# Optimization experiments

Hardware: AMD Instinct MI355X
Metric: run time of the kernel (lower is better)

The kernel has to match this reference:

```python
import jax, jax.numpy as jnp
import numpy as np

# ---- static config (mirrors module init / config constants) ----
STATE_DIM = 512
D_H = 2048
INPUT_DIM = 1024
N_QUBITS = 6
N_VQC_LAYERS = 3
MSD = 128                 # mamba_state_dim (last dim of padded state)
PAD_SLICES = 16           # padded slice count in h_padded
MIN_T = 1e-6              # control_limits.min_value
REL_STEP = 0.1            # control_limits.hardware_relative_step
ABS_STEP = 1e-4           # control_limits.hardware_absolute_step
MAX_T = 0.05              # control_limits.max_value
DIM = 2 ** N_QUBITS

# qubit 0 = most significant bit (matches reshape-based gate application)
_BITS = ((np.arange(DIM)[:, None] >> np.arange(N_QUBITS)[None, ::-1]) & 1).astype(np.float32)
_sign = np.ones(DIM, np.float32)
for k in range(N_QUBITS):  # ring CZ entanglement
    k2 = (k + 1) % N_QUBITS
    _sign *= 1.0 - 2.0 * _BITS[:, k] * _BITS[:, k2]
CZ_SIGN = jnp.asarray(_sign)
Z_OBS = jnp.asarray((1.0 - 2.0 * _BITS).mean(axis=1))  # mean <Z_k> observable weights


def _apply_ry(state, ang, k):
    # state: [B, 2^n] real statevector; ang: [B] rotation angle on qubit k
    B = state.shape[0]
    s = state.reshape(B, 2 ** k, 2, 2 ** (N_QUBITS - k - 1))
    c = jnp.cos(ang / 2)[:, None, None]
    si = jnp.sin(ang / 2)[:, None, None]
    a0, a1 = s[:, :, 0, :], s[:, :, 1, :]
    out = jnp.stack([c * a0 - si * a1, si * a0 + c * a1], axis=2)
    return out.reshape(B, DIM)


def _vqc(feats, enc_W, enc_b, thetas):
    # EvolutionTimeVQCLayer: angle-encode features, layered RY + ring CZ, mean-Z expectation
    B = feats.shape[0]
    angles = feats @ enc_W + enc_b  # [B, n_qubits]
    state = jnp.zeros((B, DIM), feats.dtype).at[:, 0].set(1.0)
    for k in range(N_QUBITS):
        state = _apply_ry(state, angles[:, k], k)
    for l in range(N_VQC_LAYERS):
        for k in range(N_QUBITS):
            state = _apply_ry(state, jnp.broadcast_to(thetas[l, k], (B,)), k)
        state = state * CZ_SIGN[None, :]
    return (state * state) @ Z_OBS  # [B]


def _hamiltonian(q, p, x, W1, b1, W2, b2, W3, b3):
    z = jnp.concatenate([q, p, x], axis=-1)          # [B, 2*S + D]
    h1 = jnp.tanh(z @ W1 + b1)
    h2 = jnp.tanh(h1 @ W2 + b2)
    return (h2 @ W3)[:, 0] + b3                       # [B] scalar energy per sample


def setup_inputs() -> dict:
    key = jax.random.key(0)
    ks = jax.random.split(key, 12)
    def glorot(k, shape):
        std = np.sqrt(2.0 / (shape[0] + shape[-1]))
        return jax.random.normal(k, shape, jnp.float32) * std
    B = 2048
    h_in = 2 * STATE_DIM + INPUT_DIM
    gen_in = INPUT_DIM + 2 * STATE_DIM
    return {
        'x': jax.random.normal(ks[0], (B, INPUT_DIM), jnp.float32),
        'h_padded': jax.random.normal(ks[1], (B, PAD_SLICES, MSD), jnp.float32),
        'aux_padded': jnp.zeros((B, PAD_SLICES, MSD), jnp.float32),
        'W1': glorot(ks[2], (h_in, D_H)), 'b1': jnp.zeros((D_H,), jnp.float32),
        'W2': glorot(ks[3], (D_H, D_H)), 'b2': jnp.zeros((D_H,), jnp.float32),
        'W3': glorot(ks[4], (D_H, 1)), 'b3': jnp.zeros((), jnp.float32),
        'W_out': glorot(ks[5], (2 * STATE_DIM, INPUT_DIM)),
        'b_out': jnp.zeros((INPUT_DIM,), jnp.float32),
        'enc_W': glorot(ks[6], (gen_in, N_QUBITS)) * 0.1,
        'enc_b': jnp.zeros((N_QUBITS,), jnp.float32),
        'thetas': jax.random.normal(ks[7], (N_VQC_LAYERS, N_QUBITS), jnp.float32) * 0.1,
        'gain': jnp.asarray(0.1, jnp.float32),
        'shift': jnp.asarray(7.0, jnp.float32),
        'cap_param': jnp.asarray(0.02, jnp.float32),
        'time_bias': jnp.asarray(0.0005, jnp.float32),
        'last_stable': jnp.asarray(0.0005, jnp.float32),
    }


def reference(x, h_padded, aux_padded, W1, b1, W2, b2, W3, b3, W_out, b_out,
              enc_W, enc_b, thetas, gain, shift, cap_param, time_bias, last_stable):
    B = x.shape[0]
    total = 2 * STATE_DIM
    num_slices = total // MSD
    # unpack phase-space state from padded mamba-shaped state
    unpacked = h_padded[:, :num_slices, :].reshape(B, total)
    q_t, p_t = jnp.split(unpacked, 2, axis=-1)

    # ---- evolution-time generation via VQC ----
    ctrl = jnp.concatenate([x, q_t, p_t], axis=-1)
    samples = _vqc(ctrl, enc_W, enc_b, thetas)                       # [B]
    soft_gain = jax.nn.softplus(gain)
    soft_shift = jax.nn.softplus(shift)
    adjusted = jax.nn.softplus(soft_gain * samples - soft_shift)
    raw = jnp.mean(adjusted) + time_bias
    cap = jnp.maximum(jax.nn.softplus(cap_param), 1e-6)
    evo = cap * jax.nn.sigmoid(raw / cap)
    evo = jnp.where(jnp.isfinite(evo), evo, cap * jax.nn.sigmoid(time_bias / cap))
    prev = jnp.maximum(last_stable, MIN_T)
    cand = jnp.maximum(evo, MIN_T)
    max_step = jnp.maximum(prev * REL_STEP, ABS_STEP)
    cand = jnp.minimum(cand, prev + max_step)
    cand = jnp.minimum(cand, MAX_T)
    dt = jnp.where(jnp.isfinite(cand), cand, prev)                   # scalar

    # ---- fused HNN symplectic (leapfrog) step ----
    def H_sum(q, p):
        return _hamiltonian(q, p, x, W1, b1, W2, b2, W3, b3).sum()
    grad_qp = jax.grad(H_sum, argnums=(0, 1))
    dHdq0, _ = grad_qp(q_t, p_t)
    p_half = p_t - 0.5 * dt * dHdq0
    _, dHdp_h = grad_qp(q_t, p_half)
    q_next = q_t + dt * dHdp_h
    dHdq_n, _ = grad_qp(q_next, p_half)
    p_next = p_half - 0.5 * dt * dHdq_n

    out = jnp.concatenate([q_next, p_next], axis=-1) @ W_out + b_out  # [B, INPUT_DIM]

    # repack state into padded mamba layout
    new_slices = jnp.concatenate([q_next, p_next], axis=-1).reshape(B, num_slices, MSD)
    pad = jnp.zeros((B, PAD_SLICES - num_slices, MSD), out.dtype)
    h_next = jnp.concatenate([new_slices, pad], axis=1)
    return out, h_next
```

## Files before the change

kernel.cpp:

```cpp
#include <hip/hip_runtime.h>
#include <math.h>

#define NB 2048
#define ZD 2048
#define SD 512
#define NELEM_Z (NB * ZD)
#define MB_ (1024 * 1024)

typedef float f32x4 __attribute__((ext_vector_type(4)));
typedef __bf16 bf16x8 __attribute__((ext_vector_type(8)));
typedef __bf16 bf16x4 __attribute__((ext_vector_type(4)));
typedef int i32x4 __attribute__((ext_vector_type(4)));
typedef int i32x8 __attribute__((ext_vector_type(8)));
typedef long long i64;

__device__ __forceinline__ float softplus_f(float x) {
  if (x > 20.f) return x;
  if (x < -20.f) return expf(x);
  return log1pf(expf(x));
}

__device__ __forceinline__ void gload_lds16(const __bf16* g, __bf16* l) {
  __builtin_amdgcn_global_load_lds(
      (__attribute__((address_space(1))) void*)(g),
      (__attribute__((address_space(3))) void*)(l), 16, 0, 0);
}

__device__ __forceinline__ int pack_fp8x4(float a, float b, float c, float d) {
  int p = __builtin_amdgcn_cvt_pk_fp8_f32(a, b, 0, false);
  p = __builtin_amdgcn_cvt_pk_fp8_f32(c, d, p, true);
  return p;
}
__device__ __forceinline__ float fp8_to_f32(unsigned char b) {
  return __builtin_amdgcn_cvt_f32_fp8((int)b, 0);
}

__global__ __launch_bounds__(256) void build_z_kernel(
    const float* __restrict__ x,
    const float* __restrict__ h_padded,
    const float* __restrict__ enc_W,
    const float* __restrict__ enc_b,
    float* __restrict__ z,
    __bf16* __restrict__ zb,
    unsigned char* __restrict__ zf8,
    float* __restrict__ angles) {
  int b = blockIdx.x;
  int tid = threadIdx.x;
  int lane = tid & 63, w = tid >> 6;
  __shared__ float red[4][6];

  float pa[6] = {0.f, 0.f, 0.f, 0.f, 0.f, 0.f};
#pragma unroll
  for (int cc = 0; cc < 2; cc++) {
    int c = cc * 256 + tid;
    int i = c * 4;
    f32x4 v = (i < 1024) ? ((const f32x4*)(h_padded + (size_t)b * 2048))[c]
                         : ((const f32x4*)(x + (size_t)b * 1024))[c - 256];
    size_t zi = (size_t)b * 512 + c;
    if (cc == 0) {
      ((f32x4*)z)[zi] = v;
      bf16x4 o;
      o[0] = (__bf16)v[0]; o[1] = (__bf16)v[1];
      o[2] = (__bf16)v[2]; o[3] = (__bf16)v[3];
      ((bf16x4*)zb)[zi] = o;
    }
    ((int*)zf8)[zi] = pack_fp8x4(v[0], v[1], v[2], v[3]);
    int cj = (i < 1024) ? (1024 + i) : (i - 1024);
#pragma unroll
    for (int e = 0; e < 4; e++) {
      const float* wp = enc_W + (size_t)(cj + e) * 6;
#pragma unroll
      for (int k = 0; k < 6; k++) pa[k] += v[e] * wp[k];
    }
  }
#pragma unroll
  for (int k = 0; k < 6; k++)
    for (int off = 32; off > 0; off >>= 1) pa[k] += __shfl_down(pa[k], off, 64);
  if (lane == 0) {
#pragma unroll
    for (int k = 0; k < 6; k++) red[w][k] = pa[k];
  }
  __syncthreads();
  if (tid < 6)
    angles[b * 6 + tid] =
        red[0][tid] + red[1][tid] + red[2][tid] + red[3][tid] + enc_b[tid];
}

__global__ void prep_w(const float* __restrict__ in,
                       __bf16* __restrict__ outT, int R, int C) {
  __shared__ float tile[32][33];
  int bx = blockIdx.x * 32, by = blockIdx.y * 32;
  int tx = threadIdx.x, ty = threadIdx.y;
  for (int r = ty; r < 32; r += 8)
    tile[r][tx] = in[(size_t)(by + r) * C + bx + tx];
  __syncthreads();
  for (int r = ty; r < 32; r += 8)
    outT[(size_t)(bx + r) * R + by + tx] = (__bf16)tile[tx][r];
}

__global__ void prep_w8(const float* __restrict__ in,
                        unsigned char* __restrict__ outN,
                        unsigned char* __restrict__ outT, int R, int C) {
  __shared__ float tile[32][33];
  int bx = blockIdx.x * 32, by = blockIdx.y * 32;
  int tx = threadIdx.x, ty = threadIdx.y;
  for (int r = ty; r < 32; r += 8) {
    float v = in[(size_t)(by + r) * C + bx + tx] * 16.f;
    tile[r][tx] = v;
    int p = __builtin_amdgcn_cvt_pk_fp8_f32(v, v, 0, false);
    outN[(size_t)(by + r) * C + bx + tx] = (unsigned char)(p & 0xff);
  }
  __syncthreads();
  for (int r = ty; r < 32; r += 8) {
    float v = tile[tx][r];
    int p = __builtin_amdgcn_cvt_pk_fp8_f32(v, v, 0, false);
    outT[(size_t)(bx + r) * R + by + tx] = (unsigned char)(p & 0xff);
  }
}

__global__ __launch_bounds__(256) void sim_kernel(
    const float* __restrict__ angles,
    const float* __restrict__ thetas,
    const float* __restrict__ gain,
    const float* __restrict__ shift,
    float* __restrict__ partial) {
  const int lane = threadIdx.x & 63;
  const int wv = threadIdx.x >> 6;
  const int row = blockIdx.x * 4 + wv;

  const int rot = ((lane << 1) | (lane >> 5)) & 63;
  const float czs = (__popc(lane & rot) & 1) ? -1.f : 1.f;
  const float zo = (6.f - 2.f * (float)__popc(lane)) * (1.f / 6.f);

  float ang = 0.f;
  if (lane < 6) ang = angles[row * 6 + lane];
  else if (lane < 24) ang = thetas[lane - 6];
  float half = 0.5f * ang;
  float cj = cosf(half), sj = sinf(half);

  float c_arr[24], s_arr[24];
#pragma unroll
  for (int j = 0; j < 24; j++) {
    c_arr[j] = __shfl(cj, j, 64);
    s_arr[j] = __shfl(sj, j, 64);
  }

  float s = (lane == 0) ? 1.f : 0.f;
#pragma unroll
  for (int j = 0; j < 24; j++) {
    const int m = 1 << (5 - (j % 6));
    float t = __shfl_xor(s, m, 64);
    float tt = (lane & m) ? t : -t;
    s = fmaf(c_arr[j], s, s_arr[j] * tt);
    if (j >= 6 && (j % 6) == 5) s *= czs;
  }

  float val = s * s * zo;
#pragma unroll
  for (int off = 32; off > 0; off >>= 1) val += __shfl_xor(val, off, 64);

  __shared__ float red[4];
  if (lane == 0) {
    float sg = softplus_f(gain[0]);
    float ss = softplus_f(shift[0]);
    red[wv] = softplus_f(sg * val - ss);
  }
  __syncthreads();
  if (threadIdx.x == 0)
    partial[blockIdx.x] = red[0] + red[1] + red[2] + red[3];
}

__global__ __launch_bounds__(256) void dt_kernel(
    const float* __restrict__ partial,
    const float* __restrict__ cap_param,
    const float* __restrict__ time_bias,
    const float* __restrict__ last_stable,
    float* __restrict__ dt_out) {
  int tid = threadIdx.x;
  int lane = tid & 63, wv = tid >> 6;
  float v = partial[tid] + partial[tid + 256];
#pragma unroll
  for (int off = 32; off > 0; off >>= 1) v += __shfl_xor(v, off, 64);
  __shared__ float red[4];
  if (lane == 0) red[wv] = v;
  __syncthreads();
  if (tid == 0) {
    float a = red[0] + red[1] + red[2] + red[3];
    float raw = a * (1.f / (float)NB) + time_bias[0];
    float cap = fmaxf(softplus_f(cap_param[0]), 1e-6f);
    float evo = cap / (1.f + expf(-raw / cap));
    if (!isfinite(evo)) evo = cap / (1.f + expf(-time_bias[0] / cap));
    float prev = fmaxf(last_stable[0], 1e-6f);
    float cand = fmaxf(evo, 1e-6f);
    float max_step = fmaxf(prev * 0.1f, 1e-4f);
    cand = fminf(cand, prev + max_step);
    cand = fminf(cand, 0.05f);
    dt_out[0] = isfinite(cand) ? cand : prev;
  }
}

template <int EPI>
__global__ __launch_bounds__(256, 2) void mfma_gemm8(
    const unsigned char* __restrict__ A, int lda,
    const unsigned char* __restrict__ Bt, int ldb,
    void* __restrict__ Cv, int ldc,
    const float* __restrict__ bias,
    const float* __restrict__ w3,
    const unsigned char* __restrict__ aux, int ldaux,
    int Kslice) {
  __shared__ __align__(16) unsigned char sA[2][128 * 128];
  __shared__ __align__(16) unsigned char sB[2][64 * 128];

  const int tid = threadIdx.x;
  const int lane = tid & 63;
  const int w = tid >> 6;
  const int wm = w & 1, wn = w >> 1;
  const int row0 = blockIdx.y * 128;
  const int col0 = blockIdx.x * 64;
  const int koff = blockIdx.z * Kslice;

  const unsigned char* gA[4]; int wA[4];
  const unsigned char* gB[2]; int wB[2];
#pragma unroll
  for (int i = 0; i < 4; i++) {
    int c = i * 256 + tid;
    int m = c >> 3, s = c & 7;
    gA[i] = A + (size_t)(row0 + m) * lda + koff + s * 16;
    wA[i] = m * 128 + ((s ^ (m & 7)) << 4);
  }
#pragma unroll
  for (int i = 0; i < 2; i++) {
    int c = i * 256 + tid;
    int m = c >> 3, s = c & 7;
    gB[i] = Bt + (size_t)(col0 + m) * ldb + koff + s * 16;
    wB[i] = m * 128 + ((s ^ (m & 7)) << 4);
  }

  const int q = lane >> 4, r = lane & 15;
  int aoff[4][2], boff[2][2];
#pragma unroll
  for (int i = 0; i < 4; i++) {
    int ma = wm * 64 + i * 16 + r;
#pragma unroll
    for (int H = 0; H < 2; H++)
      aoff[i][H] = ma * 128 + (((2 * q + H) ^ (ma & 7)) << 4);
  }
#pragma unroll
  for (int j = 0; j < 2; j++) {
    int mb = wn * 32 + j * 16 + r;
#pragma unroll
    for (int H = 0; H < 2; H++)
      boff[j][H] = mb * 128 + (((2 * q + H) ^ (mb & 7)) << 4);
  }

  f32x4 acc[4][2] = {};
  f32x4 rA[4], rB[2];

#pragma unroll
  for (int i = 0; i < 4; i++) rA[i] = *(const f32x4*)gA[i];
#pragma unroll
  for (int i = 0; i < 2; i++) rB[i] = *(const f32x4*)gB[i];
#pragma unroll
  for (int i = 0; i < 4; i++) *(f32x4*)(&sA[0][0] + wA[i]) = rA[i];
#pragma unroll
  for (int i = 0; i < 2; i++) *(f32x4*)(&sB[0][0] + wB[i]) = rB[i];
  __syncthreads();

  int cur = 0;
  for (int k0 = 0; k0 < Kslice; k0 += 128) {
    const bool more = (k0 + 128 < Kslice);
    if (more) {
#pragma unroll
      for (int i = 0; i < 4; i++) rA[i] = *(const f32x4*)(gA[i] + k0 + 128);
#pragma unroll
      for (int i = 0; i < 2; i++) rB[i] = *(const f32x4*)(gB[i] + k0 + 128);
    }

    const unsigned char* bA = &sA[cur][0];
    const unsigned char* bB = &sB[cur][0];
    i32x8 af[4], bfr[2];
#pragma unroll
    for (int i = 0; i < 4; i++) {
      i32x4 lo = *(const i32x4*)(bA + aoff[i][0]);
      i32x4 hi = *(const i32x4*)(bA + aoff[i][1]);
      af[i] = __builtin_shufflevector(lo, hi, 0, 1, 2, 3, 4, 5, 6, 7);
    }
#pragma unroll
    for (int j = 0; j < 2; j++) {
      i32x4 lo = *(const i32x4*)(bB + boff[j][0]);
      i32x4 hi = *(const i32x4*)(bB + boff[j][1]);
      bfr[j] = __builtin_shufflevector(lo, hi, 0, 1, 2, 3, 4, 5, 6, 7);
    }
#pragma unroll
    for (int i = 0; i < 4; i++)
#pragma unroll
      for (int j = 0; j < 2; j++)
        acc[i][j] = __builtin_amdgcn_mfma_scale_f32_16x16x128_f8f6f4(
            af[i], bfr[j], acc[i][j], 0 , 0 ,
            0, 0x7F7F7F7F, 0, 0x7F7F7F7F);

    if (more) {
      unsigned char* nA = &sA[cur ^ 1][0];
      unsigned char* nB = &sB[cur ^ 1][0];
#pragma unroll
      for (int i = 0; i < 4; i++) *(f32x4*)(nA + wA[i]) = rA[i];
#pragma unroll
      for (int i = 0; i < 2; i++) *(f32x4*)(nB + wB[i]) = rB[i];
    }
    __syncthreads();
    cur ^= 1;
  }

  float* Cf = (float*)Cv;
  unsigned char* C8 = (unsigned char*)Cv;
  float* Pz = Cf + (size_t)blockIdx.z * (size_t)gridDim.y * 128 * ldc;

#pragma unroll
  for (int i = 0; i < 4; i++) {
    int rowb = row0 + wm * 64 + i * 16 + q * 4;
#pragma unroll
    for (int j = 0; j < 2; j++) {
      int col = col0 + wn * 32 + j * 16 + r;
      if (EPI == 0) {
#pragma unroll
        for (int g = 0; g < 4; g++)
          Pz[(size_t)(rowb + g) * ldc + col] = acc[i][j][g];
      } else {
        float o[4];
#pragma unroll
        for (int g = 0; g < 4; g++) {
          float v = acc[i][j][g] * 0.0625f;
          if (EPI == 1) {
            o[g] = tanhf(v + bias[col]);
          } else if (EPI == 2) {
            float t = tanhf(v + bias[col]);
            o[g] = 32.f * (1.f - t * t) * w3[col];
          } else {
            float h = fp8_to_f32(aux[(size_t)(rowb + g) * ldaux + col]);
            o[g] = v * (1.f - h * h);
          }
        }
        int p = pack_fp8x4(o[0], o[1], o[2], o[3]);
#pragma unroll
        for (int g = 0; g < 4; g++)
          C8[(size_t)(rowb + g) * ldc + col] =
              (unsigned char)((p >> (8 * g)) & 0xff);
      }
    }
  }
}

__global__ __launch_bounds__(256, 2) void mfma_gemm_bf16(
    const __bf16* __restrict__ A, int lda,
    const __bf16* __restrict__ Bt, int ldb,
    float* __restrict__ P, int ldc,
    int Kslice) {
  __shared__ __bf16 sA[2][128 * 64];
  __shared__ __bf16 sB[2][64 * 64];

  const int tid = threadIdx.x;
  const int lane = tid & 63;
  const int w = tid >> 6;
  const int wm = w & 1, wn = w >> 1;
  const int row0 = blockIdx.y * 128;
  const int col0 = blockIdx.x * 64;
  const int koff = blockIdx.z * Kslice;

  const __bf16* gA[4]; int lofA[4];
  const __bf16* gB[2]; int lofB[2];
#pragma unroll
  for (int i = 0; i < 4; i++) {
    int c = i * 256 + tid;
    int m = c >> 3, cc = c & 7;
    int o = cc ^ (m & 7);
    gA[i] = A + (size_t)(row0 + m) * lda + koff + o * 8;
    lofA[i] = c * 8;
  }
#pragma unroll
  for (int i = 0; i < 2; i++) {
    int c = i * 256 + tid;
    int m = c >> 3, cc = c & 7;
    int o = cc ^ (m & 7);
    gB[i] = Bt + (size_t)(col0 + m) * ldb + koff + o * 8;
    lofB[i] = c * 8;
  }

  const int q = lane >> 4, r = lane & 15;
  int aoff[4][2], boff[2][2];
#pragma unroll
  for (int i = 0; i < 4; i++) {
    int ma = wm * 64 + i * 16 + r;
#pragma unroll
    for (int h = 0; h < 2; h++)
      aoff[i][h] = (ma * 8 + ((h * 4 + q) ^ (ma & 7))) * 8;
  }
#pragma unroll
  for (int j = 0; j < 2; j++) {
    int mb = wn * 32 + j * 16 + r;
#pragma unroll
    for (int h = 0; h < 2; h++)
      boff[j][h] = (mb * 8 + ((h * 4 + q) ^ (mb & 7))) * 8;
  }

  f32x4 acc[4][2] = {};

#pragma unroll
  for (int i = 0; i < 4; i++) gload_lds16(gA[i], &sA[0][0] + lofA[i]);
#pragma unroll
  for (int i = 0; i < 2; i++) gload_lds16(gB[i], &sB[0][0] + lofB[i]);

  int cur = 0;
  for (int k0 = 0; k0 < Kslice; k0 += 64) {
    __syncthreads();
    if (k0 + 64 < Kslice) {
      int nxt = cur ^ 1;
#pragma unroll
      for (int i = 0; i < 4; i++)
        gload_lds16(gA[i] + k0 + 64, &sA[nxt][0] + lofA[i]);
#pragma unroll
      for (int i = 0; i < 2; i++)
        gload_lds16(gB[i] + k0 + 64, &sB[nxt][0] + lofB[i]);
    }
#pragma unroll
    for (int h = 0; h < 2; h++) {
      bf16x8 af[4], bfr[2];
#pragma unroll
      for (int i = 0; i < 4; i++)
        af[i] = *(const bf16x8*)(&sA[cur][0] + aoff[i][h]);
#pragma unroll
      for (int j = 0; j < 2; j++)
        bfr[j] = *(const bf16x8*)(&sB[cur][0] + boff[j][h]);
#pragma unroll
      for (int i = 0; i < 4; i++)
#pragma unroll
        for (int j = 0; j < 2; j++)
          acc[i][j] = __builtin_amdgcn_mfma_f32_16x16x32_bf16(af[i], bfr[j],
                                                              acc[i][j], 0, 0, 0);
    }
    cur ^= 1;
  }

  float* Pz = P + (size_t)blockIdx.z * (size_t)gridDim.y * 128 * ldc;
#pragma unroll
  for (int i = 0; i < 4; i++) {
    int rowb = row0 + wm * 64 + i * 16 + q * 4;
#pragma unroll
    for (int j = 0; j < 2; j++) {
      int col = col0 + wn * 32 + j * 16 + r;
#pragma unroll
      for (int g = 0; g < 4; g++)
        Pz[(size_t)(rowb + g) * ldc + col] = acc[i][j][g];
    }
  }
}

__global__ void update_kernel(float* __restrict__ z, __bf16* __restrict__ zb,
                              unsigned char* __restrict__ zf8,
                              const float* __restrict__ gp,
                              const float* __restrict__ dt,
                              float coef, int off,
                              float* __restrict__ hout) {
  int t = blockIdx.x * blockDim.x + threadIdx.x;
  int b = t >> 7;
  int j4 = t & 127;
  const f32x4* g4 = (const f32x4*)gp;
  constexpr int STRIDE = NB * SD / 4;
  f32x4 g = g4[t] + g4[t + STRIDE] + g4[t + 2 * STRIDE] + g4[t + 3 * STRIDE];
  int zi4 = (b * ZD + off) / 4 + j4;
  f32x4 v = ((f32x4*)z)[zi4];
  float s = coef * dt[0] * (1.f / 512.f);
  v[0] += s * g[0]; v[1] += s * g[1]; v[2] += s * g[2]; v[3] += s * g[3];
  ((f32x4*)z)[zi4] = v;
  bf16x4 o;
  o[0] = (__bf16)v[0]; o[1] = (__bf16)v[1];
  o[2] = (__bf16)v[2]; o[3] = (__bf16)v[3];
  ((bf16x4*)zb)[zi4] = o;
  ((int*)zf8)[zi4] = pack_fp8x4(v[0], v[1], v[2], v[3]);
  if (hout) {
    ((f32x4*)hout)[b * 512 + (off >> 2) + j4] = v;
  }
}

__global__ void wout_reduce(const float* __restrict__ gp,
                            const float* __restrict__ b_out,
                            float* __restrict__ out) {
  int t = blockIdx.x * blockDim.x + threadIdx.x;
  constexpr int S = NB * 1024 / 4;
  const f32x4* g4 = (const f32x4*)gp;
  f32x4 v = g4[t] + g4[t + S];
  f32x4 bb = ((const f32x4*)b_out)[t & 255];
  v[0] += bb[0]; v[1] += bb[1]; v[2] += bb[2]; v[3] += bb[3];
  ((f32x4*)out)[t] = v;
}

__global__ void hzero_kernel(float* __restrict__ out) {
  int t = blockIdx.x * blockDim.x + threadIdx.x;
  int b = t >> 8;
  int j4 = t & 255;
  f32x4 zero = {0.f, 0.f, 0.f, 0.f};
  ((f32x4*)out)[b * 512 + 256 + j4] = zero;
}

extern "C" void kernel_launch(void* const* d_in, const int* in_sizes, int n_in,
                              void* d_out, int out_size, void* d_ws,
                              size_t ws_size, hipStream_t stream) {
  const float* x        = (const float*)d_in[0];
  const float* h_padded = (const float*)d_in[1];
  const float* W1    = (const float*)d_in[3];
  const float* b1    = (const float*)d_in[4];
  const float* W2    = (const float*)d_in[5];
  const float* b2    = (const float*)d_in[6];
  const float* W3    = (const float*)d_in[7];
  const float* W_out = (const float*)d_in[9];
  const float* b_out = (const float*)d_in[10];
  const float* enc_W = (const float*)d_in[11];
  const float* enc_b = (const float*)d_in[12];
  const float* thetas = (const float*)d_in[13];
  const float* gain   = (const float*)d_in[14];
  const float* shift  = (const float*)d_in[15];
  const float* cap_p  = (const float*)d_in[16];
  const float* t_bias = (const float*)d_in[17];
  const float* l_stab = (const float*)d_in[18];

  float* out_mat  = (float*)d_out;
  float* out_hnxt = (float*)d_out + NB * 1024;

  char* base = (char*)d_ws;
  float* z      = (float*)(base);
  float* part   = (float*)(base + 16 * MB_);
  __bf16* zb    = (__bf16*)(base + 32 * MB_);
  __bf16* Wot   = (__bf16*)(base + 40 * MB_);
  float* angl   = (float*)(base + 42 * MB_);
  float* dtp    = (float*)(base + 42 * MB_ + 65536);
  float* simp   = (float*)(base + 42 * MB_ + 80 * 1024);
  unsigned char* zf8  = (unsigned char*)(base + 43 * MB_);
  unsigned char* h1_8 = zf8 + (size_t)NELEM_Z;
  unsigned char* g2_8 = h1_8 + (size_t)NELEM_Z;
  unsigned char* g1_8 = g2_8 + (size_t)NELEM_Z;
  unsigned char* W1n8 = g1_8 + (size_t)NELEM_Z;
  unsigned char* W1t8 = W1n8 + (size_t)NELEM_Z;
  unsigned char* W2n8 = W1t8 + (size_t)NELEM_Z;
  unsigned char* W2t8 = W2n8 + (size_t)NELEM_Z;

  dim3 thr256(256);
  dim3 thrT(32, 8);

  prep_w8<<<dim3(64, 64), thrT, 0, stream>>>(W1, W1n8, W1t8, ZD, ZD);
  prep_w8<<<dim3(64, 64), thrT, 0, stream>>>(W2, W2n8, W2t8, ZD, ZD);
  prep_w<<<dim3(32, 32), thrT, 0, stream>>>(W_out, Wot, 1024, 1024);

  build_z_kernel<<<dim3(NB), thr256, 0, stream>>>(x, h_padded, enc_W, enc_b, z,
                                                  zb, zf8, angl);
  sim_kernel<<<dim3(NB / 4), thr256, 0, stream>>>(angl, thetas, gain, shift,
                                                  simp);
  dt_kernel<<<dim3(1), thr256, 0, stream>>>(simp, cap_p, t_bias, l_stab, dtp);
  hzero_kernel<<<dim3(NB * 1024 / 4 / 256), thr256, 0, stream>>>(out_hnxt);

  const int   j0r[3]  = {0, 512, 0};
  const int   offs[3] = {512, 0, 512};
  const float coef[3] = {-0.5f, 1.0f, -0.5f};
  float* houts[3];
  houts[0] = nullptr;
  houts[1] = out_hnxt;
  houts[2] = out_hnxt;

  dim3 gridSq(32, 16, 1);
  dim3 gridGr(8, 16, 4);

  for (int i = 0; i < 3; i++) {
    mfma_gemm8<1><<<gridSq, thr256, 0, stream>>>(
        zf8, ZD, W1t8, ZD, h1_8, ZD, b1, nullptr, nullptr, 0, ZD);
    mfma_gemm8<2><<<gridSq, thr256, 0, stream>>>(
        h1_8, ZD, W2t8, ZD, g2_8, ZD, b2, W3, nullptr, 0, ZD);
    mfma_gemm8<3><<<gridSq, thr256, 0, stream>>>(
        g2_8, ZD, W2n8, ZD, g1_8, ZD, nullptr, nullptr, h1_8, ZD, ZD);
    mfma_gemm8<0><<<gridGr, thr256, 0, stream>>>(
        g1_8, ZD, W1n8 + (size_t)j0r[i] * ZD, ZD, part, SD, nullptr, nullptr,
        nullptr, 0, 512);
    update_kernel<<<dim3(NB * SD / 4 / 256), thr256, 0, stream>>>(
        z, zb, zf8, part, dtp, coef[i], offs[i], houts[i]);
  }

  mfma_gemm_bf16<<<dim3(16, 16, 2), thr256, 0, stream>>>(zb, ZD, Wot, 1024,
                                                         part, 1024, 512);
  wout_reduce<<<dim3(NB * 1024 / 4 / 256), thr256, 0, stream>>>(part, b_out,
                                                                out_mat);
}
```

Baseline: 409.3 us.

## Use direct global-to-LDS async loads in fp8 GEMM and merge weight prep launches

```diff
diff --git a/kernel.cpp b/kernel.cpp
--- a/kernel.cpp
+++ b/kernel.cpp
@@ -21,6 +21,12 @@
 }
 
 __device__ __forceinline__ void gload_lds16(const __bf16* g, __bf16* l) {
+  __builtin_amdgcn_global_load_lds(
+      (__attribute__((address_space(1))) void*)(g),
+      (__attribute__((address_space(3))) void*)(l), 16, 0, 0);
+}
+__device__ __forceinline__ void gload_lds16u(const unsigned char* g,
+                                             unsigned char* l) {
   __builtin_amdgcn_global_load_lds(
       (__attribute__((address_space(1))) void*)(g),
       (__attribute__((address_space(3))) void*)(l), 16, 0, 0);
@@ -98,9 +104,16 @@
     outT[(size_t)(bx + r) * R + by + tx] = (__bf16)tile[tx][r];
 }
 
-__global__ void prep_w8(const float* __restrict__ in,
-                        unsigned char* __restrict__ outN,
-                        unsigned char* __restrict__ outT, int R, int C) {
+__global__ void prep_w8x2(const float* __restrict__ W1,
+                          const float* __restrict__ W2,
+                          unsigned char* __restrict__ N1,
+                          unsigned char* __restrict__ T1,
+                          unsigned char* __restrict__ N2,
+                          unsigned char* __restrict__ T2) {
+  const float* in = blockIdx.z ? W2 : W1;
+  unsigned char* outN = blockIdx.z ? N2 : N1;
+  unsigned char* outT = blockIdx.z ? T2 : T1;
+  const int C = ZD, R = ZD;
   __shared__ float tile[32][33];
   int bx = blockIdx.x * 32, by = blockIdx.y * 32;
   int tx = threadIdx.x, ty = threadIdx.y;
@@ -219,21 +232,23 @@
   const int col0 = blockIdx.x * 64;
   const int koff = blockIdx.z * Kslice;
 
-  const unsigned char* gA[4]; int wA[4];
-  const unsigned char* gB[2]; int wB[2];
+  const unsigned char* gA[4]; int dA[4];
+  const unsigned char* gB[2]; int dB[2];
 #pragma unroll
   for (int i = 0; i < 4; i++) {
     int c = i * 256 + tid;
     int m = c >> 3, s = c & 7;
-    gA[i] = A + (size_t)(row0 + m) * lda + koff + s * 16;
-    wA[i] = m * 128 + ((s ^ (m & 7)) << 4);
+    int l = s ^ (m & 7);
+    gA[i] = A + (size_t)(row0 + m) * lda + koff + l * 16;
+    dA[i] = c * 16;
   }
 #pragma unroll
   for (int i = 0; i < 2; i++) {
     int c = i * 256 + tid;
     int m = c >> 3, s = c & 7;
-    gB[i] = Bt + (size_t)(col0 + m) * ldb + koff + s * 16;
-    wB[i] = m * 128 + ((s ^ (m & 7)) << 4);
+    int l = s ^ (m & 7);
+    gB[i] = Bt + (size_t)(col0 + m) * ldb + koff + l * 16;
+    dB[i] = c * 16;
   }
 
   const int q = lane >> 4, r = lane & 15;
@@ -254,26 +269,23 @@
   }
 
   f32x4 acc[4][2] = {};
-  f32x4 rA[4], rB[2];
-
-#pragma unroll
-  for (int i = 0; i < 4; i++) rA[i] = *(const f32x4*)gA[i];
-#pragma unroll
-  for (int i = 0; i < 2; i++) rB[i] = *(const f32x4*)gB[i];
-#pragma unroll
-  for (int i = 0; i < 4; i++) *(f32x4*)(&sA[0][0] + wA[i]) = rA[i];
-#pragma unroll
-  for (int i = 0; i < 2; i++) *(f32x4*)(&sB[0][0] + wB[i]) = rB[i];
-  __syncthreads();
+
+#pragma unroll
+  for (int i = 0; i < 4; i++) gload_lds16u(gA[i], &sA[0][0] + dA[i]);
+#pragma unroll
+  for (int i = 0; i < 2; i++) gload_lds16u(gB[i], &sB[0][0] + dB[i]);
 
   int cur = 0;
   for (int k0 = 0; k0 < Kslice; k0 += 128) {
-    const bool more = (k0 + 128 < Kslice);
-    if (more) {
-#pragma unroll
-      for (int i = 0; i < 4; i++) rA[i] = *(const f32x4*)(gA[i] + k0 + 128);
-#pragma unroll
-      for (int i = 0; i < 2; i++) rB[i] = *(const f32x4*)(gB[i] + k0 + 128);
+    __syncthreads();
+    if (k0 + 128 < Kslice) {
+      int nxt = cur ^ 1;
+#pragma unroll
+      for (int i = 0; i < 4; i++)
+        gload_lds16u(gA[i] + k0 + 128, &sA[nxt][0] + dA[i]);
+#pragma unroll
+      for (int i = 0; i < 2; i++)
+        gload_lds16u(gB[i] + k0 + 128, &sB[nxt][0] + dB[i]);
     }
 
     const unsigned char* bA = &sA[cur][0];
@@ -298,16 +310,6 @@
         acc[i][j] = __builtin_amdgcn_mfma_scale_f32_16x16x128_f8f6f4(
             af[i], bfr[j], acc[i][j], 0 , 0 ,
             0, 0x7F7F7F7F, 0, 0x7F7F7F7F);
-
-    if (more) {
-      unsigned char* nA = &sA[cur ^ 1][0];
-      unsigned char* nB = &sB[cur ^ 1][0];
-#pragma unroll
-      for (int i = 0; i < 4; i++) *(f32x4*)(nA + wA[i]) = rA[i];
-#pragma unroll
-      for (int i = 0; i < 2; i++) *(f32x4*)(nB + wB[i]) = rB[i];
-    }
-    __syncthreads();
     cur ^= 1;
   }
 
@@ -545,8 +547,8 @@
   dim3 thr256(256);
   dim3 thrT(32, 8);
 
-  prep_w8<<<dim3(64, 64), thrT, 0, stream>>>(W1, W1n8, W1t8, ZD, ZD);
-  prep_w8<<<dim3(64, 64), thrT, 0, stream>>>(W2, W2n8, W2t8, ZD, ZD);
+  prep_w8x2<<<dim3(64, 64, 2), thrT, 0, stream>>>(W1, W2, W1n8, W1t8, W2n8,
+                                                  W2t8);
   prep_w<<<dim3(32, 32), thrT, 0, stream>>>(W_out, Wot, 1024, 1024);
 
   build_z_kernel<<<dim3(NB), thr256, 0, stream>>>(x, h_padded, enc_W, enc_b, z,
```

Result: no change. 412.5 us (+0.8%).
